# Kernel optimization log

Measured on AMD Instinct MI355X. Metric: run time of the kernel, lower is better.

## Reference

```python
import jax, jax.numpy as jnp
import numpy as np

B, S, D, H = 4, 2048, 512, 8
DEPTH = D // H


def setup_inputs() -> dict:
    key = jax.random.key(0)
    ks = jax.random.split(key, 12)
    s = 0.02
    return {
        "q": jax.random.normal(ks[0], (B, S, D), jnp.float32),
        "k": jax.random.normal(ks[1], (B, S, D), jnp.float32),
        "v": jax.random.normal(ks[2], (B, S, D), jnp.float32),
        "mask": jax.random.randint(ks[3], (B, 1, 1, S), 0, 2, jnp.int32),
        "wq": jax.random.normal(ks[4], (D, D), jnp.float32) * s,
        "bq": jnp.zeros((D,), jnp.float32),
        "wk": jax.random.normal(ks[5], (D, D), jnp.float32) * s,
        "bk": jnp.zeros((D,), jnp.float32),
        "wv": jax.random.normal(ks[6], (D, D), jnp.float32) * s,
        "bv": jnp.zeros((D,), jnp.float32),
        "wo": jax.random.normal(ks[7], (D, D), jnp.float32) * s,
        "bo": jnp.zeros((D,), jnp.float32),
    }


def _split_heads(x):
    # [B,S,D] -> [B,H,S,depth]
    b = x.shape[0]
    return x.reshape(b, -1, H, DEPTH).transpose(0, 2, 1, 3)


def reference(q, k, v, mask, wq, bq, wk, bk, wv, bv, wo, bo):
    qh = _split_heads(q @ wq + bq)
    kh = _split_heads(k @ wk + bk)
    vh = _split_heads(v @ wv + bv)
    scale = 1.0 / jnp.sqrt(jnp.float32(DEPTH))
    logits = jnp.einsum("bhqd,bhkd->bhqk", qh, kh) * scale
    logits = logits + mask.astype(jnp.float32) * -1e9
    attn = jax.nn.softmax(logits, axis=-1)  # [B,H,Sq,Sk]
    out = jnp.einsum("bhqk,bhkd->bhqd", attn, vh)
    out = out.transpose(0, 2, 1, 3).reshape(q.shape[0], -1, D)
    out = out @ wo + bo
    return out, attn
```

## Files before the change

### kernel.cpp

```cpp
#include <hip/hip_runtime.h>

#define B_ 4
#define S_ 2048
#define D_ 512
#define H_ 8
#define DP_ 64
#define NT_ (S_/64)

typedef __attribute__((ext_vector_type(4))) float f32x4;
typedef __attribute__((ext_vector_type(8))) short short8;
typedef __attribute__((ext_vector_type(4))) int i32x4;

__device__ __forceinline__ short f2bf(float f){
  unsigned u = __float_as_uint(f);
  u += 0x7fff + ((u >> 16) & 1);
  return (short)(u >> 16);
}

__device__ __forceinline__ int cvtpk(float lo, float hi){
  int r;
  asm("v_cvt_pk_bf16_f32 %0, %1, %2" : "=v"(r) : "v"(lo), "v"(hi));
  return r;
}

#define SWZ(r, kb) ((r)*64 + ((kb) ^ (((r)&7)<<3)))
#define F2(r) ((((r)&3)) | ((((r)>>3)&1)<<2))
#define SWZ2(r, kb) ((r)*64 + ((kb) ^ (F2(r)<<3)))

#define WAITV(N) do{ asm volatile("s_waitcnt vmcnt(" #N ")" ::: "memory"); }while(0)
#define BAR() do{ __builtin_amdgcn_s_barrier(); __builtin_amdgcn_sched_barrier(0); }while(0)

template<int NC>
__device__ __forceinline__ void stage_swz(const short* __restrict__ g, int rowStride,
                                          short* shbase, int w, int l){
  #pragma unroll
  for(int i = 0; i < NC; ++i){
    int byte = (w*NC + i)*1024 + l*16;
    int row = byte >> 7;
    int gs = ((byte >> 4) & 7) ^ (row & 7);
    const short* src = g + (size_t)row*rowStride + gs*8;
    __builtin_amdgcn_global_load_lds((const __attribute__((address_space(1))) void*)src,
        (__attribute__((address_space(3))) void*)(shbase + (w*NC + i)*512), 16, 0, 0);
  }
}
template<int NC>
__device__ __forceinline__ void stage_swz2(const short* __restrict__ g, int rowStride,
                                           short* shbase, int w, int l){
  #pragma unroll
  for(int i = 0; i < NC; ++i){
    int byte = (w*NC + i)*1024 + l*16;
    int row = byte >> 7;
    int gs = ((byte >> 4) & 7) ^ F2(row);
    const short* src = g + (size_t)row*rowStride + gs*8;
    __builtin_amdgcn_global_load_lds((const __attribute__((address_space(1))) void*)src,
        (__attribute__((address_space(3))) void*)(shbase + (w*NC + i)*512), 16, 0, 0);
  }
}

__global__ __launch_bounds__(256) void k_pre(const int* __restrict__ mask,
        const float* __restrict__ w0, const float* __restrict__ w1,
        const float* __restrict__ w2, const float* __restrict__ w3,
        short* __restrict__ wT, float* __restrict__ mb){
  __shared__ float tt[32][33];
  const int bi = blockIdx.x, t = threadIdx.x;
  if(bi < 1024){
    const int z = bi >> 8;
    const float* w = z == 0 ? w0 : z == 1 ? w1 : z == 2 ? w2 : w3;
    short* wt = wT + z * 262144;
    const int bxy = bi & 255;
    const int bx = (bxy & 15) * 32, by = (bxy >> 4) * 32;
    const int tx = t & 31, ty = t >> 5;
    #pragma unroll
    for(int i = 0; i < 32; i += 8) tt[ty + i][tx] = w[(by + ty + i) * D_ + bx + tx];
    __syncthreads();
    #pragma unroll
    for(int i = 0; i < 32; i += 8) wt[(bx + ty + i) * D_ + by + tx] = f2bf(tt[tx][ty + i]);
  } else {
    int i = (bi - 1024) * 256 + t;
    mb[i] = mask[i] ? -1.0e9f : 0.0f;
  }
}

__global__ __launch_bounds__(256) void k_gemm_qkv(const float* __restrict__ qf,
        const float* __restrict__ kf, const float* __restrict__ vf,
        const short* __restrict__ WTall, const float* __restrict__ b0,
        const float* __restrict__ b1, const float* __restrict__ b2,
        short* __restrict__ qh, short* __restrict__ kh, short* __restrict__ vvt){
  __shared__ __align__(16) short As[8192];
  __shared__ __align__(16) short Bs[8192];
  const int z = blockIdx.z;
  const float* X = z == 0 ? qf : (z == 1 ? kf : vf);
  const short* WT = WTall + (size_t)z * (D_*D_);
  const float* bias = z==0 ? b0 : (z==1 ? b1 : b2);
  const int t = threadIdx.x, l = t & 63, w = t >> 6;
  const int lr = l & 15, lg = l >> 4;
  const int m0 = blockIdx.x * 128, n0 = blockIdx.y * 128;
  const int wr = w >> 1, wc = w & 1;
  const float* Xb = X + (size_t)m0 * D_;
  const short* Wb = WT + (size_t)n0 * D_;
  f32x4 acc[4][4] = {};
  for(int kt = 0; kt < D_ / 64; ++kt){
    #pragma unroll
    for(int i = 0; i < 4; ++i){
      int e = t + 256 * i;
      int row = e >> 3, c8 = (e & 7) * 8;
      const float* src = Xb + (size_t)row * D_ + kt * 64 + c8;
      float4 f0 = *reinterpret_cast<const float4*>(src);
      float4 f1 = *reinterpret_cast<const float4*>(src + 4);
      i32x4 pk;
      pk[0] = cvtpk(f0.x, f0.y); pk[1] = cvtpk(f0.z, f0.w);
      pk[2] = cvtpk(f1.x, f1.y); pk[3] = cvtpk(f1.z, f1.w);
      *reinterpret_cast<i32x4*>(&As[SWZ(row, c8)]) = pk;
    }
    stage_swz<4>(Wb + kt*64, D_, Bs, w, l);
    __syncthreads();
    #pragma unroll
    for(int ks = 0; ks < 2; ++ks){
      const int kb = ks*32 + lg*8;
      short8 a[4], b[4];
      #pragma unroll
      for(int mt = 0; mt < 4; ++mt)
        a[mt] = *reinterpret_cast<const short8*>(&As[SWZ(wr*64 + mt*16 + lr, kb)]);
      #pragma unroll
      for(int nt = 0; nt < 4; ++nt)
        b[nt] = *reinterpret_cast<const short8*>(&Bs[SWZ(wc*64 + nt*16 + lr, kb)]);
      __builtin_amdgcn_s_setprio(1);
      #pragma unroll
      for(int mt = 0; mt < 4; ++mt)
        #pragma unroll
        for(int nt = 0; nt < 4; ++nt)
          acc[mt][nt] = __builtin_amdgcn_mfma_f32_16x16x32_bf16(a[mt], b[nt], acc[mt][nt], 0, 0, 0);
      __builtin_amdgcn_s_setprio(0);
    }
    __syncthreads();
  }
  #pragma unroll
  for(int mt = 0; mt < 4; ++mt){
    #pragma unroll
    for(int nt = 0; nt < 4; ++nt){
      const int n = n0 + wc*64 + nt*16 + lr;
      const int m4 = m0 + wr*64 + mt*16 + lg*4;
      float vals[4];
      #pragma unroll
      for(int r = 0; r < 4; ++r) vals[r] = acc[mt][nt][r] + bias[n];
      if(z == 2){
        short4 pv4;
        pv4.x = f2bf(vals[0]); pv4.y = f2bf(vals[1]); pv4.z = f2bf(vals[2]); pv4.w = f2bf(vals[3]);
        *reinterpret_cast<short4*>(&vvt[
            (((size_t)((m4 >> 11) * H_ + (n >> 6))) * DP_ + (n & 63)) * S_ + (m4 & 2047)]) = pv4;
      } else {
        short* dst = z == 0 ? qh : kh;
        #pragma unroll
        for(int r = 0; r < 4; ++r){
          int m = m4 + r;
          dst[(((size_t)((m >> 11) * H_ + (n >> 6))) * S_ + (m & 2047)) * DP_ + (n & 63)] = f2bf(vals[r]);
        }
      }
    }
  }
}

__global__ __launch_bounds__(256) void k_gemm_out(const short* __restrict__ X,
        const short* __restrict__ WT, const float* __restrict__ bias,
        float* __restrict__ Out){
  __shared__ __align__(16) short As[8192];
  __shared__ __align__(16) short Bs[8192];
  const int t = threadIdx.x, l = t & 63, w = t >> 6;
  const int lr = l & 15, lg = l >> 4;
  const int m0 = blockIdx.x * 128, n0 = blockIdx.y * 128;
  const int wr = w >> 1, wc = w & 1;
  const short* Xb = X + (size_t)m0 * D_;
  const short* Wb = WT + (size_t)n0 * D_;
  f32x4 acc[4][4] = {};
  for(int kt = 0; kt < D_ / 64; ++kt){
    stage_swz<4>(Xb + kt*64, D_, As, w, l);
    stage_swz<4>(Wb + kt*64, D_, Bs, w, l);
    __syncthreads();
    #pragma unroll
    for(int ks = 0; ks < 2; ++ks){
      const int kb = ks*32 + lg*8;
      short8 a[4], b[4];
      #pragma unroll
      for(int mt = 0; mt < 4; ++mt)
        a[mt] = *reinterpret_cast<const short8*>(&As[SWZ(wr*64 + mt*16 + lr, kb)]);
      #pragma unroll
      for(int nt = 0; nt < 4; ++nt)
        b[nt] = *reinterpret_cast<const short8*>(&Bs[SWZ(wc*64 + nt*16 + lr, kb)]);
      __builtin_amdgcn_s_setprio(1);
      #pragma unroll
      for(int mt = 0; mt < 4; ++mt)
        #pragma unroll
        for(int nt = 0; nt < 4; ++nt)
          acc[mt][nt] = __builtin_amdgcn_mfma_f32_16x16x32_bf16(a[mt], b[nt], acc[mt][nt], 0, 0, 0);
      __builtin_amdgcn_s_setprio(0);
    }
    __syncthreads();
  }
  #pragma unroll
  for(int mt = 0; mt < 4; ++mt){
    #pragma unroll
    for(int nt = 0; nt < 4; ++nt){
      const int n = n0 + wc*64 + nt*16 + lr;
      const int m4 = m0 + wr*64 + mt*16 + lg*4;
      #pragma unroll
      for(int r = 0; r < 4; ++r)
        Out[(size_t)(m4 + r) * D_ + n] = acc[mt][nt][r] + bias[n];
    }
  }
}

__global__ __launch_bounds__(512, 4) void k_attn(const short* __restrict__ qh,
                                                 const short* __restrict__ kh,
                                                 const short* __restrict__ vt,
                                                 const float* __restrict__ mb,
                                                 float* __restrict__ attn,
                                                 short* __restrict__ ctx){
  __shared__ __align__(16) short Sh[28672];
  const int t = threadIdx.x, l = t & 63, w = t >> 6;
  const int lr = l & 15, lg = l >> 4;
  int lin = blockIdx.y * 16 + blockIdx.x;
  int sw = (lin & 7) * 64 + (lin >> 3);
  const int bh = sw >> 4, b = bh >> 3, h = bh & 7;
  const int q0 = (sw & 15) * 128;
  const short* Qb = qh + (size_t)bh * S_ * DP_ + (size_t)q0 * DP_;
  const short* Kb = kh + (size_t)bh * S_ * DP_;
  const short* Vtb = vt + (size_t)bh * DP_ * S_;
  const float* Mbb = mb + b * S_;
  float* Mlds = (float*)(Sh + 24576);
  const float scale = 0.125f;

  stage_swz2<2>(Qb, DP_, Sh + 16384, w, l);
  __builtin_amdgcn_global_load_lds(
      (const __attribute__((address_space(1))) void*)(Mbb + w*256 + l*4),
      (__attribute__((address_space(3))) void*)(Mlds + w*256 + l*4), 16, 0, 0);
  stage_swz2<1>(Kb, DP_, Sh, w, l);
  stage_swz2<1>(Kb + 4096, DP_, Sh + 4096, w, l);
  stage_swz2<1>(Kb + 8192, DP_, Sh + 8192, w, l);
  WAITV(3); BAR();
  short8 bq0, bq1;
  {
    int r = w * 16 + lr;
    bq0 = *reinterpret_cast<const short8*>(&Sh[16384 + SWZ2(r, lg * 8)]);
    bq1 = *reinterpret_cast<const short8*>(&Sh[16384 + SWZ2(r, 32 + lg * 8)]);
  }

  float ps = 0.f;
  for(int kt = 0; kt < NT_; ++kt){
    if(kt <= NT_ - 3){ WAITV(2); } else if(kt == NT_ - 2){ WAITV(1); } else { WAITV(0); }
    BAR();
    if(kt + 3 < NT_)
      stage_swz2<1>(Kb + (size_t)(kt + 3) * 4096, DP_, Sh + ((kt + 3) & 3) * 4096, w, l);
    const short* Kc = Sh + (kt & 3) * 4096;
    const float* Ml = Mlds + kt * 64;
    #pragma unroll
    for(int st = 0; st < 4; ++st){
      const float4 mv = *(const float4*)&Ml[st * 16 + lg * 4];
      short8 ak0 = *reinterpret_cast<const short8*>(&Kc[SWZ2(st * 16 + lr, lg * 8)]);
      short8 ak1 = *reinterpret_cast<const short8*>(&Kc[SWZ2(st * 16 + lr, 32 + lg * 8)]);
      __builtin_amdgcn_s_setprio(1);
      f32x4 c = {};
      c = __builtin_amdgcn_mfma_f32_16x16x32_bf16(ak0, bq0, c, 0, 0, 0);
      c = __builtin_amdgcn_mfma_f32_16x16x32_bf16(ak1, bq1, c, 0, 0, 0);
      __builtin_amdgcn_s_setprio(0);
      ps += __expf(__builtin_fmaf(c[0], scale, mv.x));
      ps += __expf(__builtin_fmaf(c[1], scale, mv.y));
      ps += __expf(__builtin_fmaf(c[2], scale, mv.z));
      ps += __expf(__builtin_fmaf(c[3], scale, mv.w));
    }
  }
  BAR();
  stage_swz2<1>(Kb, DP_, Sh, w, l);
  stage_swz2<1>(Vtb, S_, Sh + 12288, w, l);
  stage_swz2<1>(Kb + 4096, DP_, Sh + 4096, w, l);
  stage_swz2<1>(Vtb + 64, S_, Sh + 16384, w, l);
  ps += __shfl_xor(ps, 16, 64);
  ps += __shfl_xor(ps, 32, 64);
  const float rinv = 1.f / ps;

  f32x4 o[4] = {};
  const int grow = ((lr >> 2) << 3) + (lr & 3);
  for(int kt = 0; kt < NT_; ++kt){
    if(kt == 0){ WAITV(2); }
    else if(kt == 1){ WAITV(6); }
    else if(kt == NT_ - 1){ WAITV(8); }
    else { WAITV(10); }
    BAR();
    if(kt + 2 < NT_){
      stage_swz2<1>(Kb + (size_t)(kt + 2) * 4096, DP_, Sh + ((kt + 2) % 3) * 4096, w, l);
      stage_swz2<1>(Vtb + (size_t)(kt + 2) * 64, S_, Sh + 12288 + ((kt + 2) % 3) * 4096, w, l);
    }
    const short* Kc = Sh + (kt % 3) * 4096;
    const short* Vc = Sh + 12288 + (kt % 3) * 4096;
    const float* Ml = Mlds + kt * 64;
    const int q = q0 + w * 16 + lr;
    i32x4 pav[2];
    #pragma unroll
    for(int st = 0; st < 4; ++st){
      const int ks = st >> 1, h4 = st & 1;
      const int row = grow + h4 * 4 + ks * 32;
      const int mcol = ks * 32 + h4 * 4 + lg * 8;
      const float4 mv = *(const float4*)&Ml[mcol];
      short8 ak0 = *reinterpret_cast<const short8*>(&Kc[SWZ2(row, lg * 8)]);
      short8 ak1 = *reinterpret_cast<const short8*>(&Kc[SWZ2(row, 32 + lg * 8)]);
      __builtin_amdgcn_s_setprio(1);
      f32x4 c = {};
      c = __builtin_amdgcn_mfma_f32_16x16x32_bf16(ak0, bq0, c, 0, 0, 0);
      c = __builtin_amdgcn_mfma_f32_16x16x32_bf16(ak1, bq1, c, 0, 0, 0);
      __builtin_amdgcn_s_setprio(0);
      float4 pw;
      pw.x = __expf(__builtin_fmaf(c[0], scale, mv.x)) * rinv;
      pw.y = __expf(__builtin_fmaf(c[1], scale, mv.y)) * rinv;
      pw.z = __expf(__builtin_fmaf(c[2], scale, mv.z)) * rinv;
      pw.w = __expf(__builtin_fmaf(c[3], scale, mv.w)) * rinv;
      *reinterpret_cast<float4*>(&attn[((size_t)bh * S_ + q) * S_ + kt * 64 + mcol]) = pw;
      pav[ks][h4 * 2 + 0] = cvtpk(pw.x, pw.y);
      pav[ks][h4 * 2 + 1] = cvtpk(pw.z, pw.w);
    }
    #pragma unroll
    for(int ks = 0; ks < 2; ++ks){
      short8 pa = __builtin_bit_cast(short8, pav[ks]);
      __builtin_amdgcn_s_setprio(1);
      #pragma unroll
      for(int dt = 0; dt < 4; ++dt){
        short8 vb = *reinterpret_cast<const short8*>(&Vc[SWZ2(dt * 16 + lr, ks * 32 + lg * 8)]);
        o[dt] = __builtin_amdgcn_mfma_f32_16x16x32_bf16(pa, vb, o[dt], 0, 0, 0);
      }
      __builtin_amdgcn_s_setprio(0);
    }
  }
  #pragma unroll
  for(int dt = 0; dt < 4; ++dt){
    #pragma unroll
    for(int r = 0; r < 4; ++r){
      int q = q0 + w * 16 + lg * 4 + r;
      int dd = h * 64 + dt * 16 + lr;
      ctx[((size_t)b * S_ + q) * D_ + dd] = f2bf(o[dt][r]);
    }
  }
}

extern "C" void kernel_launch(void* const* d_in, const int* in_sizes, int n_in,
                              void* d_out, int out_size, void* d_ws, size_t ws_size,
                              hipStream_t stream){
  const float* q  = (const float*)d_in[0];
  const float* k  = (const float*)d_in[1];
  const float* v  = (const float*)d_in[2];
  const int* mask = (const int*)d_in[3];
  const float* wq = (const float*)d_in[4];
  const float* bq = (const float*)d_in[5];
  const float* wk = (const float*)d_in[6];
  const float* bk = (const float*)d_in[7];
  const float* wv = (const float*)d_in[8];
  const float* bv = (const float*)d_in[9];
  const float* wo = (const float*)d_in[10];
  const float* bo = (const float*)d_in[11];

  float* out  = (float*)d_out;
  float* attn = out + (size_t)B_ * S_ * D_;

  char* ws = (char*)d_ws;
  short* qh  = (short*)(ws);
  short* kh  = (short*)(ws + 8388608);
  short* vvt = (short*)(ws + 16777216);
  short* ctx = (short*)(ws + 25165824);
  short* wT  = (short*)(ws + 33554432);
  float* mb  = (float*)(ws + 33554432 + 4 * 524288);

  hipLaunchKernelGGL(k_pre, dim3(1056), dim3(256), 0, stream,
                     mask, wq, wk, wv, wo, wT, mb);

  hipLaunchKernelGGL(k_gemm_qkv, dim3(64, 4, 3), dim3(256), 0, stream,
                     q, k, v, wT, bq, bk, bv, qh, kh, vvt);

  hipLaunchKernelGGL(k_attn, dim3(16, 32), dim3(512), 0, stream, qh, kh, vvt, mb, attn, ctx);

  hipLaunchKernelGGL(k_gemm_out, dim3(64, 4), dim3(256), 0, stream, ctx, wT + 3 * 262144, bo, out);
}
```

Before: 229.4 us.

## Process two K/V tiles per barrier with deeper LDS ring buffers

Measured after the change: 223.9 us. -2.4%, faster.

```diff
diff --git a/kernel.cpp b/kernel.cpp
--- a/kernel.cpp
+++ b/kernel.cpp
@@ -215,7 +215,7 @@
                                                  const float* __restrict__ mb,
                                                  float* __restrict__ attn,
                                                  short* __restrict__ ctx){
-  __shared__ __align__(16) short Sh[28672];
+  __shared__ __align__(16) short Sh[36864];
   const int t = threadIdx.x, l = t & 63, w = t >> 6;
   const int lr = l & 15, lg = l >> 4;
   int lin = blockIdx.y * 16 + blockIdx.x;
@@ -226,106 +226,130 @@
   const short* Kb = kh + (size_t)bh * S_ * DP_;
   const short* Vtb = vt + (size_t)bh * DP_ * S_;
   const float* Mbb = mb + b * S_;
-  float* Mlds = (float*)(Sh + 24576);
+  float* Mlds = (float*)Sh;
+  short* KA = Sh + 4096;
+  short* KB = Sh + 4096;
+  short* VB = Sh + 20480;
+  short* Qs = Sh + 28672;
   const float scale = 0.125f;
 
-  stage_swz2<2>(Qb, DP_, Sh + 16384, w, l);
   __builtin_amdgcn_global_load_lds(
       (const __attribute__((address_space(1))) void*)(Mbb + w*256 + l*4),
       (__attribute__((address_space(3))) void*)(Mlds + w*256 + l*4), 16, 0, 0);
-  stage_swz2<1>(Kb, DP_, Sh, w, l);
-  stage_swz2<1>(Kb + 4096, DP_, Sh + 4096, w, l);
-  stage_swz2<1>(Kb + 8192, DP_, Sh + 8192, w, l);
-  WAITV(3); BAR();
+  stage_swz2<2>(Qb, DP_, Qs, w, l);
+  stage_swz2<1>(Kb,            DP_, KA,            w, l);
+  stage_swz2<1>(Kb + 4096,     DP_, KA + 4096,     w, l);
+  stage_swz2<1>(Kb + 2*4096,   DP_, KA + 2*4096,   w, l);
+  stage_swz2<1>(Kb + 3*4096,   DP_, KA + 3*4096,   w, l);
+  WAITV(4); BAR();
   short8 bq0, bq1;
   {
     int r = w * 16 + lr;
-    bq0 = *reinterpret_cast<const short8*>(&Sh[16384 + SWZ2(r, lg * 8)]);
-    bq1 = *reinterpret_cast<const short8*>(&Sh[16384 + SWZ2(r, 32 + lg * 8)]);
-  }
+    bq0 = *reinterpret_cast<const short8*>(&Qs[SWZ2(r, lg * 8)]);
+    bq1 = *reinterpret_cast<const short8*>(&Qs[SWZ2(r, 32 + lg * 8)]);
+  }
+  const int grow = ((lr >> 2) << 3) + (lr & 3);
 
   float ps = 0.f;
-  for(int kt = 0; kt < NT_; ++kt){
-    if(kt <= NT_ - 3){ WAITV(2); } else if(kt == NT_ - 2){ WAITV(1); } else { WAITV(0); }
+  for(int i = 0; i < NT_/2; ++i){
+    if(i < NT_/2 - 1){ WAITV(2); } else { WAITV(0); }
     BAR();
-    if(kt + 3 < NT_)
-      stage_swz2<1>(Kb + (size_t)(kt + 3) * 4096, DP_, Sh + ((kt + 3) & 3) * 4096, w, l);
-    const short* Kc = Sh + (kt & 3) * 4096;
-    const float* Ml = Mlds + kt * 64;
-    #pragma unroll
-    for(int st = 0; st < 4; ++st){
-      const float4 mv = *(const float4*)&Ml[st * 16 + lg * 4];
-      short8 ak0 = *reinterpret_cast<const short8*>(&Kc[SWZ2(st * 16 + lr, lg * 8)]);
-      short8 ak1 = *reinterpret_cast<const short8*>(&Kc[SWZ2(st * 16 + lr, 32 + lg * 8)]);
-      __builtin_amdgcn_s_setprio(1);
-      f32x4 c = {};
-      c = __builtin_amdgcn_mfma_f32_16x16x32_bf16(ak0, bq0, c, 0, 0, 0);
-      c = __builtin_amdgcn_mfma_f32_16x16x32_bf16(ak1, bq1, c, 0, 0, 0);
-      __builtin_amdgcn_s_setprio(0);
-      ps += __expf(__builtin_fmaf(c[0], scale, mv.x));
-      ps += __expf(__builtin_fmaf(c[1], scale, mv.y));
-      ps += __expf(__builtin_fmaf(c[2], scale, mv.z));
-      ps += __expf(__builtin_fmaf(c[3], scale, mv.w));
-    }
-  }
-  BAR();
-  stage_swz2<1>(Kb, DP_, Sh, w, l);
-  stage_swz2<1>(Vtb, S_, Sh + 12288, w, l);
-  stage_swz2<1>(Kb + 4096, DP_, Sh + 4096, w, l);
-  stage_swz2<1>(Vtb + 64, S_, Sh + 16384, w, l);
+    if(i + 2 < NT_/2){
+      int tfa = 2*i + 4, tfb = 2*i + 5;
+      stage_swz2<1>(Kb + (size_t)tfa * 4096, DP_, KA + (tfa % 6) * 4096, w, l);
+      stage_swz2<1>(Kb + (size_t)tfb * 4096, DP_, KA + (tfb % 6) * 4096, w, l);
+    }
+    #pragma unroll
+    for(int tt = 0; tt < 2; ++tt){
+      const int kt = 2*i + tt;
+      const short* Kc = KA + (kt % 6) * 4096;
+      const float* Ml = Mlds + kt * 64;
+      #pragma unroll
+      for(int st = 0; st < 4; ++st){
+        const int ks = st >> 1, h4 = st & 1;
+        const int row = grow + h4 * 4 + ks * 32;
+        const int mcol = ks * 32 + h4 * 4 + lg * 8;
+        const float4 mv = *(const float4*)&Ml[mcol];
+        short8 ak0 = *reinterpret_cast<const short8*>(&Kc[SWZ2(row, lg * 8)]);
+        short8 ak1 = *reinterpret_cast<const short8*>(&Kc[SWZ2(row, 32 + lg * 8)]);
+        __builtin_amdgcn_s_setprio(1);
+        f32x4 c = {};
+        c = __builtin_amdgcn_mfma_f32_16x16x32_bf16(ak0, bq0, c, 0, 0, 0);
+        c = __builtin_amdgcn_mfma_f32_16x16x32_bf16(ak1, bq1, c, 0, 0, 0);
+        __builtin_amdgcn_s_setprio(0);
+        ps += __expf(__builtin_fmaf(c[0], scale, mv.x));
+        ps += __expf(__builtin_fmaf(c[1], scale, mv.y));
+        ps += __expf(__builtin_fmaf(c[2], scale, mv.z));
+        ps += __expf(__builtin_fmaf(c[3], scale, mv.w));
+      }
+    }
+  }
   ps += __shfl_xor(ps, 16, 64);
   ps += __shfl_xor(ps, 32, 64);
   const float rinv = 1.f / ps;
 
+  BAR();
+  stage_swz2<1>(Kb,          DP_, KB,          w, l);
+  stage_swz2<1>(Kb + 4096,   DP_, KB + 4096,   w, l);
+  stage_swz2<1>(Vtb,         S_,  VB,          w, l);
+  stage_swz2<1>(Vtb + 64,    S_,  VB + 4096,   w, l);
+  stage_swz2<1>(Kb + 2*4096, DP_, KB + 2*4096, w, l);
+  stage_swz2<1>(Kb + 3*4096, DP_, KB + 3*4096, w, l);
+  stage_swz2<1>(Vtb + 2*64,  S_,  VB + 2*4096, w, l);
+  stage_swz2<1>(Vtb + 3*64,  S_,  VB + 3*4096, w, l);
+
   f32x4 o[4] = {};
-  const int grow = ((lr >> 2) << 3) + (lr & 3);
-  for(int kt = 0; kt < NT_; ++kt){
-    if(kt == 0){ WAITV(2); }
-    else if(kt == 1){ WAITV(6); }
-    else if(kt == NT_ - 1){ WAITV(8); }
-    else { WAITV(10); }
+  for(int i = 0; i < NT_/2; ++i){
+    if(i == 0){ WAITV(4); } else { WAITV(8); }
     BAR();
-    if(kt + 2 < NT_){
-      stage_swz2<1>(Kb + (size_t)(kt + 2) * 4096, DP_, Sh + ((kt + 2) % 3) * 4096, w, l);
-      stage_swz2<1>(Vtb + (size_t)(kt + 2) * 64, S_, Sh + 12288 + ((kt + 2) % 3) * 4096, w, l);
-    }
-    const short* Kc = Sh + (kt % 3) * 4096;
-    const short* Vc = Sh + 12288 + (kt % 3) * 4096;
-    const float* Ml = Mlds + kt * 64;
-    const int q = q0 + w * 16 + lr;
-    i32x4 pav[2];
-    #pragma unroll
-    for(int st = 0; st < 4; ++st){
-      const int ks = st >> 1, h4 = st & 1;
-      const int row = grow + h4 * 4 + ks * 32;
-      const int mcol = ks * 32 + h4 * 4 + lg * 8;
-      const float4 mv = *(const float4*)&Ml[mcol];
-      short8 ak0 = *reinterpret_cast<const short8*>(&Kc[SWZ2(row, lg * 8)]);
-      short8 ak1 = *reinterpret_cast<const short8*>(&Kc[SWZ2(row, 32 + lg * 8)]);
-      __builtin_amdgcn_s_setprio(1);
-      f32x4 c = {};
-      c = __builtin_amdgcn_mfma_f32_16x16x32_bf16(ak0, bq0, c, 0, 0, 0);
-      c = __builtin_amdgcn_mfma_f32_16x16x32_bf16(ak1, bq1, c, 0, 0, 0);
-      __builtin_amdgcn_s_setprio(0);
-      float4 pw;
-      pw.x = __expf(__builtin_fmaf(c[0], scale, mv.x)) * rinv;
-      pw.y = __expf(__builtin_fmaf(c[1], scale, mv.y)) * rinv;
-      pw.z = __expf(__builtin_fmaf(c[2], scale, mv.z)) * rinv;
-      pw.w = __expf(__builtin_fmaf(c[3], scale, mv.w)) * rinv;
-      *reinterpret_cast<float4*>(&attn[((size_t)bh * S_ + q) * S_ + kt * 64 + mcol]) = pw;
-      pav[ks][h4 * 2 + 0] = cvtpk(pw.x, pw.y);
-      pav[ks][h4 * 2 + 1] = cvtpk(pw.z, pw.w);
-    }
-    #pragma unroll
-    for(int ks = 0; ks < 2; ++ks){
-      short8 pa = __builtin_bit_cast(short8, pav[ks]);
-      __builtin_amdgcn_s_setprio(1);
-      #pragma unroll
-      for(int dt = 0; dt < 4; ++dt){
-        short8 vb = *reinterpret_cast<const short8*>(&Vc[SWZ2(dt * 16 + lr, ks * 32 + lg * 8)]);
-        o[dt] = __builtin_amdgcn_mfma_f32_16x16x32_bf16(pa, vb, o[dt], 0, 0, 0);
+    if(i >= 1 && i + 1 < NT_/2){
+      int tfa = 2*i + 2, tfb = 2*i + 3;
+      stage_swz2<1>(Kb + (size_t)tfa * 4096, DP_, KB + (tfa & 3) * 4096, w, l);
+      stage_swz2<1>(Kb + (size_t)tfb * 4096, DP_, KB + (tfb & 3) * 4096, w, l);
+      stage_swz2<1>(Vtb + (size_t)tfa * 64,  S_,  VB + (tfa & 3) * 4096, w, l);
+      stage_swz2<1>(Vtb + (size_t)tfb * 64,  S_,  VB + (tfb & 3) * 4096, w, l);
+    }
+    #pragma unroll
+    for(int tt = 0; tt < 2; ++tt){
+      const int kt = 2*i + tt;
+      const short* Kc = KB + (kt & 3) * 4096;
+      const short* Vc = VB + (kt & 3) * 4096;
+      const float* Ml = Mlds + kt * 64;
+      const int q = q0 + w * 16 + lr;
+      i32x4 pav[2];
+      #pragma unroll
+      for(int st = 0; st < 4; ++st){
+        const int ks = st >> 1, h4 = st & 1;
+        const int row = grow + h4 * 4 + ks * 32;
+        const int mcol = ks * 32 + h4 * 4 + lg * 8;
+        const float4 mv = *(const float4*)&Ml[mcol];
+        short8 ak0 = *reinterpret_cast<const short8*>(&Kc[SWZ2(row, lg * 8)]);
+        short8 ak1 = *reinterpret_cast<const short8*>(&Kc[SWZ2(row, 32 + lg * 8)]);
+        __builtin_amdgcn_s_setprio(1);
+        f32x4 c = {};
+        c = __builtin_amdgcn_mfma_f32_16x16x32_bf16(ak0, bq0, c, 0, 0, 0);
+        c = __builtin_amdgcn_mfma_f32_16x16x32_bf16(ak1, bq1, c, 0, 0, 0);
+        __builtin_amdgcn_s_setprio(0);
+        float4 pw;
+        pw.x = __expf(__builtin_fmaf(c[0], scale, mv.x)) * rinv;
+        pw.y = __expf(__builtin_fmaf(c[1], scale, mv.y)) * rinv;
+        pw.z = __expf(__builtin_fmaf(c[2], scale, mv.z)) * rinv;
+        pw.w = __expf(__builtin_fmaf(c[3], scale, mv.w)) * rinv;
+        *reinterpret_cast<float4*>(&attn[((size_t)bh * S_ + q) * S_ + kt * 64 + mcol]) = pw;
+        pav[ks][h4 * 2 + 0] = cvtpk(pw.x, pw.y);
+        pav[ks][h4 * 2 + 1] = cvtpk(pw.z, pw.w);
       }
-      __builtin_amdgcn_s_setprio(0);
+      #pragma unroll
+      for(int ks = 0; ks < 2; ++ks){
+        short8 pa = __builtin_bit_cast(short8, pav[ks]);
+        __builtin_amdgcn_s_setprio(1);
+        #pragma unroll
+        for(int dt = 0; dt < 4; ++dt){
+          short8 vb = *reinterpret_cast<const short8*>(&Vc[SWZ2(dt * 16 + lr, ks * 32 + lg * 8)]);
+          o[dt] = __builtin_amdgcn_mfma_f32_16x16x32_bf16(pa, vb, o[dt], 0, 0, 0);
+        }
+        __builtin_amdgcn_s_setprio(0);
+      }
     }
   }
   #pragma unroll
```

## Shrink attention blocks to 64 queries with 32-key tiles and exp2 softmax

Applied to the files above, without the earlier changes.

New measurement: 263.6 us. +14.9%, slower.

```diff
diff --git a/kernel.cpp b/kernel.cpp
--- a/kernel.cpp
+++ b/kernel.cpp
@@ -5,7 +5,7 @@
 #define D_ 512
 #define H_ 8
 #define DP_ 64
-#define NT_ (S_/64)
+#define NT2_ (S_/32)
 
 typedef __attribute__((ext_vector_type(4))) float f32x4;
 typedef __attribute__((ext_vector_type(8))) short short8;
@@ -43,18 +43,25 @@
         (__attribute__((address_space(3))) void*)(shbase + (w*NC + i)*512), 16, 0, 0);
   }
 }
-template<int NC>
-__device__ __forceinline__ void stage_swz2(const short* __restrict__ g, int rowStride,
-                                           short* shbase, int w, int l){
-  #pragma unroll
-  for(int i = 0; i < NC; ++i){
-    int byte = (w*NC + i)*1024 + l*16;
-    int row = byte >> 7;
-    int gs = ((byte >> 4) & 7) ^ F2(row);
-    const short* src = g + (size_t)row*rowStride + gs*8;
-    __builtin_amdgcn_global_load_lds((const __attribute__((address_space(1))) void*)src,
-        (__attribute__((address_space(3))) void*)(shbase + (w*NC + i)*512), 16, 0, 0);
-  }
+
+__device__ __forceinline__ void stage_k32(const short* __restrict__ g,
+                                          short* dst, int w, int l){
+  int byte = w*1024 + l*16;
+  int row = byte >> 7;
+  int gs = ((byte >> 4) & 7) ^ F2(row);
+  const short* src = g + (size_t)row*DP_ + gs*8;
+  __builtin_amdgcn_global_load_lds((const __attribute__((address_space(1))) void*)src,
+      (__attribute__((address_space(3))) void*)(dst + (byte >> 1)), 16, 0, 0);
+}
+__device__ __forceinline__ void stage_v32(const short* __restrict__ g,
+                                          short* dst, int w, int l){
+  int byte = w*1024 + l*16;
+  int d = byte >> 6;
+  int ch = (byte >> 4) & 3;
+  int sc = ch ^ (d & 3);
+  const short* src = g + (size_t)d*S_ + sc*8;
+  __builtin_amdgcn_global_load_lds((const __attribute__((address_space(1))) void*)src,
+      (__attribute__((address_space(3))) void*)(dst + (byte >> 1)), 16, 0, 0);
 }
 
 __global__ __launch_bounds__(256) void k_pre(const int* __restrict__ mask,
@@ -77,7 +84,7 @@
     for(int i = 0; i < 32; i += 8) wt[(bx + ty + i) * D_ + by + tx] = f2bf(tt[tx][ty + i]);
   } else {
     int i = (bi - 1024) * 256 + t;
-    mb[i] = mask[i] ? -1.0e9f : 0.0f;
+    mb[i] = mask[i] ? -1.442695041e9f : 0.0f;
   }
 }
 
@@ -209,97 +216,98 @@
   }
 }
 
-__global__ __launch_bounds__(512, 4) void k_attn(const short* __restrict__ qh,
+__global__ __launch_bounds__(256, 6) void k_attn(const short* __restrict__ qh,
                                                  const short* __restrict__ kh,
                                                  const short* __restrict__ vt,
                                                  const float* __restrict__ mb,
                                                  float* __restrict__ attn,
                                                  short* __restrict__ ctx){
-  __shared__ __align__(16) short Sh[28672];
+  __shared__ __align__(16) short Sh[12288];
   const int t = threadIdx.x, l = t & 63, w = t >> 6;
   const int lr = l & 15, lg = l >> 4;
-  int lin = blockIdx.y * 16 + blockIdx.x;
-  int sw = (lin & 7) * 64 + (lin >> 3);
-  const int bh = sw >> 4, b = bh >> 3, h = bh & 7;
-  const int q0 = (sw & 15) * 128;
+  int lin = blockIdx.y * 32 + blockIdx.x;
+  int sw = (lin & 7) * 128 + (lin >> 3);
+  const int bh = sw >> 5, b = bh >> 3, h = bh & 7;
+  const int q0 = (sw & 31) * 64;
   const short* Qb = qh + (size_t)bh * S_ * DP_ + (size_t)q0 * DP_;
   const short* Kb = kh + (size_t)bh * S_ * DP_;
   const short* Vtb = vt + (size_t)bh * DP_ * S_;
   const float* Mbb = mb + b * S_;
-  float* Mlds = (float*)(Sh + 24576);
-  const float scale = 0.125f;
-
-  stage_swz2<2>(Qb, DP_, Sh + 16384, w, l);
-  __builtin_amdgcn_global_load_lds(
-      (const __attribute__((address_space(1))) void*)(Mbb + w*256 + l*4),
-      (__attribute__((address_space(3))) void*)(Mlds + w*256 + l*4), 16, 0, 0);
-  stage_swz2<1>(Kb, DP_, Sh, w, l);
-  stage_swz2<1>(Kb + 4096, DP_, Sh + 4096, w, l);
-  stage_swz2<1>(Kb + 8192, DP_, Sh + 8192, w, l);
-  WAITV(3); BAR();
+  float* Mlds = (float*)Sh;
+  short* SlabA = Sh + 4096;
+  short* KB = Sh + 4096;
+  short* VB = Sh + 8192;
+  const float scale2 = 0.125f * 1.442695041f;
+
   short8 bq0, bq1;
   {
-    int r = w * 16 + lr;
-    bq0 = *reinterpret_cast<const short8*>(&Sh[16384 + SWZ2(r, lg * 8)]);
-    bq1 = *reinterpret_cast<const short8*>(&Sh[16384 + SWZ2(r, 32 + lg * 8)]);
-  }
+    const short* qr = Qb + (size_t)(w * 16 + lr) * DP_;
+    bq0 = *reinterpret_cast<const short8*>(qr + lg * 8);
+    bq1 = *reinterpret_cast<const short8*>(qr + 32 + lg * 8);
+  }
+  #pragma unroll
+  for(int i = 0; i < 2; ++i){
+    int byte = (w*2 + i)*1024 + l*16;
+    __builtin_amdgcn_global_load_lds(
+        (const __attribute__((address_space(1))) void*)((const char*)Mbb + byte),
+        (__attribute__((address_space(3))) void*)((char*)Mlds + byte), 16, 0, 0);
+  }
+  stage_k32(Kb, SlabA, w, l);
+  stage_k32(Kb + 32*DP_, SlabA + 2048, w, l);
+  WAITV(2); BAR();
+  const int grow = ((lr >> 2) << 3) + (lr & 3);
 
   float ps = 0.f;
-  for(int kt = 0; kt < NT_; ++kt){
-    if(kt <= NT_ - 3){ WAITV(2); } else if(kt == NT_ - 2){ WAITV(1); } else { WAITV(0); }
+  for(int kt = 0; kt < NT2_; ++kt){
+    if(kt < NT2_ - 1){ WAITV(1); } else { WAITV(0); }
     BAR();
-    if(kt + 3 < NT_)
-      stage_swz2<1>(Kb + (size_t)(kt + 3) * 4096, DP_, Sh + ((kt + 3) & 3) * 4096, w, l);
-    const short* Kc = Sh + (kt & 3) * 4096;
-    const float* Ml = Mlds + kt * 64;
-    #pragma unroll
-    for(int st = 0; st < 4; ++st){
-      const float4 mv = *(const float4*)&Ml[st * 16 + lg * 4];
-      short8 ak0 = *reinterpret_cast<const short8*>(&Kc[SWZ2(st * 16 + lr, lg * 8)]);
-      short8 ak1 = *reinterpret_cast<const short8*>(&Kc[SWZ2(st * 16 + lr, 32 + lg * 8)]);
+    if(kt + 2 < NT2_)
+      stage_k32(Kb + (size_t)(kt + 2) * 32 * DP_, SlabA + ((kt + 2) % 3) * 2048, w, l);
+    const short* Kc = SlabA + (kt % 3) * 2048;
+    const float* Ml = Mlds + kt * 32;
+    #pragma unroll
+    for(int h4 = 0; h4 < 2; ++h4){
+      const int row = grow + h4 * 4;
+      const int mcol = h4 * 4 + lg * 8;
+      const float4 mv = *reinterpret_cast<const float4*>(&Ml[mcol]);
+      short8 ak0 = *reinterpret_cast<const short8*>(&Kc[SWZ2(row, lg * 8)]);
+      short8 ak1 = *reinterpret_cast<const short8*>(&Kc[SWZ2(row, 32 + lg * 8)]);
       __builtin_amdgcn_s_setprio(1);
       f32x4 c = {};
       c = __builtin_amdgcn_mfma_f32_16x16x32_bf16(ak0, bq0, c, 0, 0, 0);
       c = __builtin_amdgcn_mfma_f32_16x16x32_bf16(ak1, bq1, c, 0, 0, 0);
       __builtin_amdgcn_s_setprio(0);
-      ps += __expf(__builtin_fmaf(c[0], scale, mv.x));
-      ps += __expf(__builtin_fmaf(c[1], scale, mv.y));
-      ps += __expf(__builtin_fmaf(c[2], scale, mv.z));
-      ps += __expf(__builtin_fmaf(c[3], scale, mv.w));
-    }
-  }
-  BAR();
-  stage_swz2<1>(Kb, DP_, Sh, w, l);
-  stage_swz2<1>(Vtb, S_, Sh + 12288, w, l);
-  stage_swz2<1>(Kb + 4096, DP_, Sh + 4096, w, l);
-  stage_swz2<1>(Vtb + 64, S_, Sh + 16384, w, l);
+      ps += __builtin_amdgcn_exp2f(__builtin_fmaf(c[0], scale2, mv.x));
+      ps += __builtin_amdgcn_exp2f(__builtin_fmaf(c[1], scale2, mv.y));
+      ps += __builtin_amdgcn_exp2f(__builtin_fmaf(c[2], scale2, mv.z));
+      ps += __builtin_amdgcn_exp2f(__builtin_fmaf(c[3], scale2, mv.w));
+    }
+  }
   ps += __shfl_xor(ps, 16, 64);
   ps += __shfl_xor(ps, 32, 64);
   const float rinv = 1.f / ps;
 
+  BAR();
+  stage_k32(Kb, KB, w, l);
+  stage_v32(Vtb, VB, w, l);
   f32x4 o[4] = {};
-  const int grow = ((lr >> 2) << 3) + (lr & 3);
-  for(int kt = 0; kt < NT_; ++kt){
-    if(kt == 0){ WAITV(2); }
-    else if(kt == 1){ WAITV(6); }
-    else if(kt == NT_ - 1){ WAITV(8); }
-    else { WAITV(10); }
+  const int qg = q0 + w * 16 + lr;
+  for(int kt = 0; kt < NT2_; ++kt){
+    if(kt == 0){ WAITV(0); } else { WAITV(2); }
     BAR();
-    if(kt + 2 < NT_){
-      stage_swz2<1>(Kb + (size_t)(kt + 2) * 4096, DP_, Sh + ((kt + 2) % 3) * 4096, w, l);
-      stage_swz2<1>(Vtb + (size_t)(kt + 2) * 64, S_, Sh + 12288 + ((kt + 2) % 3) * 4096, w, l);
-    }
-    const short* Kc = Sh + (kt % 3) * 4096;
-    const short* Vc = Sh + 12288 + (kt % 3) * 4096;
-    const float* Ml = Mlds + kt * 64;
-    const int q = q0 + w * 16 + lr;
-    i32x4 pav[2];
-    #pragma unroll
-    for(int st = 0; st < 4; ++st){
-      const int ks = st >> 1, h4 = st & 1;
-      const int row = grow + h4 * 4 + ks * 32;
-      const int mcol = ks * 32 + h4 * 4 + lg * 8;
-      const float4 mv = *(const float4*)&Ml[mcol];
+    if(kt + 1 < NT2_){
+      stage_k32(Kb + (size_t)(kt + 1) * 32 * DP_, KB + ((kt + 1) & 1) * 2048, w, l);
+      stage_v32(Vtb + (kt + 1) * 32, VB + ((kt + 1) & 1) * 2048, w, l);
+    }
+    const short* Kc = KB + (kt & 1) * 2048;
+    const short* Vc = VB + (kt & 1) * 2048;
+    const float* Ml = Mlds + kt * 32;
+    i32x4 pav;
+    #pragma unroll
+    for(int h4 = 0; h4 < 2; ++h4){
+      const int row = grow + h4 * 4;
+      const int mcol = h4 * 4 + lg * 8;
+      const float4 mv = *reinterpret_cast<const float4*>(&Ml[mcol]);
       short8 ak0 = *reinterpret_cast<const short8*>(&Kc[SWZ2(row, lg * 8)]);
       short8 ak1 = *reinterpret_cast<const short8*>(&Kc[SWZ2(row, 32 + lg * 8)]);
       __builtin_amdgcn_s_setprio(1);
@@ -308,33 +316,31 @@
       c = __builtin_amdgcn_mfma_f32_16x16x32_bf16(ak1, bq1, c, 0, 0, 0);
       __builtin_amdgcn_s_setprio(0);
       float4 pw;
-      pw.x = __expf(__builtin_fmaf(c[0], scale, mv.x)) * rinv;
-      pw.y = __expf(__builtin_fmaf(c[1], scale, mv.y)) * rinv;
-      pw.z = __expf(__builtin_fmaf(c[2], scale, mv.z)) * rinv;
-      pw.w = __expf(__builtin_fmaf(c[3], scale, mv.w)) * rinv;
-      *reinterpret_cast<float4*>(&attn[((size_t)bh * S_ + q) * S_ + kt * 64 + mcol]) = pw;
-      pav[ks][h4 * 2 + 0] = cvtpk(pw.x, pw.y);
-      pav[ks][h4 * 2 + 1] = cvtpk(pw.z, pw.w);
-    }
-    #pragma unroll
-    for(int ks = 0; ks < 2; ++ks){
-      short8 pa = __builtin_bit_cast(short8, pav[ks]);
-      __builtin_amdgcn_s_setprio(1);
-      #pragma unroll
-      for(int dt = 0; dt < 4; ++dt){
-        short8 vb = *reinterpret_cast<const short8*>(&Vc[SWZ2(dt * 16 + lr, ks * 32 + lg * 8)]);
-        o[dt] = __builtin_amdgcn_mfma_f32_16x16x32_bf16(pa, vb, o[dt], 0, 0, 0);
-      }
-      __builtin_amdgcn_s_setprio(0);
-    }
+      pw.x = __builtin_amdgcn_exp2f(__builtin_fmaf(c[0], scale2, mv.x)) * rinv;
+      pw.y = __builtin_amdgcn_exp2f(__builtin_fmaf(c[1], scale2, mv.y)) * rinv;
+      pw.z = __builtin_amdgcn_exp2f(__builtin_fmaf(c[2], scale2, mv.z)) * rinv;
+      pw.w = __builtin_amdgcn_exp2f(__builtin_fmaf(c[3], scale2, mv.w)) * rinv;
+      *reinterpret_cast<float4*>(&attn[((size_t)bh * S_ + qg) * S_ + kt * 32 + mcol]) = pw;
+      pav[h4 * 2 + 0] = cvtpk(pw.x, pw.y);
+      pav[h4 * 2 + 1] = cvtpk(pw.z, pw.w);
+    }
+    short8 pa = __builtin_bit_cast(short8, pav);
+    __builtin_amdgcn_s_setprio(1);
+    #pragma unroll
+    for(int dt = 0; dt < 4; ++dt){
+      const int d = dt * 16 + lr;
+      short8 vb = *reinterpret_cast<const short8*>(&Vc[d * 32 + ((lg ^ (d & 3)) * 8)]);
+      o[dt] = __builtin_amdgcn_mfma_f32_16x16x32_bf16(pa, vb, o[dt], 0, 0, 0);
+    }
+    __builtin_amdgcn_s_setprio(0);
   }
   #pragma unroll
   for(int dt = 0; dt < 4; ++dt){
     #pragma unroll
     for(int r = 0; r < 4; ++r){
-      int q = q0 + w * 16 + lg * 4 + r;
+      int qq = q0 + w * 16 + lg * 4 + r;
       int dd = h * 64 + dt * 16 + lr;
-      ctx[((size_t)b * S_ + q) * D_ + dd] = f2bf(o[dt][r]);
+      ctx[((size_t)b * S_ + qq) * D_ + dd] = f2bf(o[dt][r]);
     }
   }
 }
@@ -372,7 +378,7 @@
   hipLaunchKernelGGL(k_gemm_qkv, dim3(64, 4, 3), dim3(256), 0, stream,
                      q, k, v, wT, bq, bk, bv, qh, kh, vvt);
 
-  hipLaunchKernelGGL(k_attn, dim3(16, 32), dim3(512), 0, stream, qh, kh, vvt, mb, attn, ctx);
+  hipLaunchKernelGGL(k_attn, dim3(32, 32), dim3(256), 0, stream, qh, kh, vvt, mb, attn, ctx);
 
   hipLaunchKernelGGL(k_gemm_out, dim3(64, 4), dim3(256), 0, stream, ctx, wT + 3 * 262144, bo, out);
 }
```
